# Kernel tuning notes

Hardware: AMD Instinct MI355X
Metric: run time of the kernel (lower is better)

Reference implementation:

```python
import jax, jax.numpy as jnp
import numpy as np

DIM = 384
NUM_HEADS = 8
HEAD_DIM = DIM // NUM_HEADS
SCALE = HEAD_DIM ** -0.5
MLP_HIDDEN = int(DIM * 4.0)
EPS = 1e-6


def setup_inputs() -> dict:
    key = jax.random.key(0)
    ks = jax.random.split(key, 8)
    s = 0.02
    return {
        "x": jax.random.normal(ks[0], (2, DIM, 8, 16, 16), dtype=jnp.float32),
        "g1": jnp.ones((DIM,), jnp.float32),
        "b1": jnp.zeros((DIM,), jnp.float32),
        "Wqkv": jax.random.normal(ks[1], (DIM, 3 * DIM), jnp.float32) * s,  # no bias (qkv_bias=False)
        "Wo": jax.random.normal(ks[2], (DIM, DIM), jnp.float32) * s,
        "bo": jnp.zeros((DIM,), jnp.float32),
        "g2": jnp.ones((DIM,), jnp.float32),
        "b2": jnp.zeros((DIM,), jnp.float32),
        "W1": jax.random.normal(ks[3], (DIM, MLP_HIDDEN), jnp.float32) * s,
        "b1m": jnp.zeros((MLP_HIDDEN,), jnp.float32),
        "W2": jax.random.normal(ks[4], (MLP_HIDDEN, DIM), jnp.float32) * s,
        "b2m": jnp.zeros((DIM,), jnp.float32),
    }


def _layernorm(x, g, b):
    mu = jnp.mean(x, axis=-1, keepdims=True)
    var = jnp.mean(jnp.square(x - mu), axis=-1, keepdims=True)
    return (x - mu) * jax.lax.rsqrt(var + EPS) * g + b


def _attention(h, Wqkv, Wo, bo):
    B, N, C = h.shape
    qkv = h @ Wqkv  # [B, N, 3C]
    qkv = qkv.reshape(B, N, 3, NUM_HEADS, HEAD_DIM).transpose(2, 0, 3, 1, 4)
    q, k, v = qkv[0], qkv[1], qkv[2]  # each [B, H, N, d]
    att = jax.nn.softmax(jnp.einsum('bhxd,bhyd->bhxy', q, k) * SCALE, axis=-1)
    out = jnp.einsum('bhxy,bhyd->bhxd', att, v)  # [B, H, N, d]
    out = out.transpose(0, 2, 1, 3).reshape(B, N, C)
    return out @ Wo + bo


def reference(x, g1, b1, Wqkv, Wo, bo, g2, b2, W1, b1m, W2, b2m):
    B, C, D, H, W = x.shape
    h = x.transpose(0, 2, 3, 4, 1).reshape(B, D * H * W, C)  # b (d h w) c
    h = h + _attention(_layernorm(h, g1, b1), Wqkv, Wo, bo)
    m = _layernorm(h, g2, b2)
    m = jax.nn.gelu(m @ W1 + b1m, approximate=False) @ W2 + b2m
    h = h + m
    return h.reshape(B, D, H, W, C).transpose(0, 4, 1, 2, 3)
```

## Files before the change

### kernel.cpp

```cpp
#include <hip/hip_runtime.h>
#include <hip/hip_bf16.h>
#include <math.h>

#define DIM    384
#define NHEAD  8
#define HDIM   48
#define NTOK   2048
#define BATCH  2
#define TOKS   (BATCH * NTOK)
#define HIDDEN 1536

typedef __bf16 bf16x8 __attribute__((ext_vector_type(8)));
typedef float  f32x4  __attribute__((ext_vector_type(4)));
typedef unsigned short u16;

union bfu { __hip_bfloat16 h; u16 u; };

__device__ __forceinline__ void load_lds16(const void* g, void* l) {
    __builtin_amdgcn_global_load_lds(
        (const __attribute__((address_space(1))) void*)g,
        (__attribute__((address_space(3))) void*)l, 16, 0, 0);
}

__global__ __launch_bounds__(256) void prep(
    const float* __restrict__ Wqkv, const float* __restrict__ Wo,
    const float* __restrict__ W1,   const float* __restrict__ W2,
    __hip_bfloat16* __restrict__ WqkvT, __hip_bfloat16* __restrict__ WoT,
    __hip_bfloat16* __restrict__ W1T,   __hip_bfloat16* __restrict__ W2T,
    const float* __restrict__ x, const float* __restrict__ g,
    const float* __restrict__ bta,
    float* __restrict__ hOut, __hip_bfloat16* __restrict__ y) {
    __shared__ __align__(16) char smem[384 * 33 * 4];
    int id = blockIdx.x;
    int tid = threadIdx.x;
    if (id < 1728) {
        float (*t)[33] = (float(*)[33])smem;
        const float* src; __hip_bfloat16* dst; int R, C;
        if (id < 432)       { src = Wqkv; dst = WqkvT; R = 384;  C = 1152; }
        else if (id < 576)  { id -= 432;  src = Wo;    dst = WoT;  R = 384;  C = 384; }
        else if (id < 1152) { id -= 576;  src = W1;    dst = W1T;  R = 384;  C = 1536; }
        else                { id -= 1152; src = W2;    dst = W2T;  R = 1536; C = 384; }
        int tc = C / 32;
        int i0 = (id / tc) * 32, j0 = (id % tc) * 32;
        int tx = tid & 31, ty = tid >> 5;
#pragma unroll
        for (int k = 0; k < 32; k += 8)
            t[ty + k][tx] = src[(size_t)(i0 + ty + k) * C + j0 + tx];
        __syncthreads();
#pragma unroll
        for (int k = 0; k < 32; k += 8)
            dst[(size_t)(j0 + ty + k) * R + i0 + tx] = __float2bfloat16(t[tx][ty + k]);
    } else {
        float* t = (float*)smem;
        int id2 = id - 1728;
        int n0 = (id2 & 63) * 32, b = id2 >> 6;
        const float* xb = x + (size_t)b * DIM * NTOK;
        for (int idx = tid; idx < 384 * 32; idx += 256) {
            int c = idx >> 5, n = idx & 31;
            t[c * 33 + n] = xb[(size_t)c * NTOK + n0 + n];
        }
        __syncthreads();
        int wid = tid >> 6, lane = tid & 63;
#pragma unroll
        for (int it = 0; it < 8; ++it) {
            int tl = it * 4 + wid;
            float v[6];
            float s = 0.f;
#pragma unroll
            for (int i = 0; i < 6; ++i) { v[i] = t[(lane + 64 * i) * 33 + tl]; s += v[i]; }
#pragma unroll
            for (int o = 32; o; o >>= 1) s += __shfl_xor(s, o, 64);
            float mu = s * (1.f / DIM);
            float s2 = 0.f;
#pragma unroll
            for (int i = 0; i < 6; ++i) { float d = v[i] - mu; s2 += d * d; }
#pragma unroll
            for (int o = 32; o; o >>= 1) s2 += __shfl_xor(s2, o, 64);
            float r = rsqrtf(s2 * (1.f / DIM) + 1e-6f);
            size_t tok = (size_t)b * NTOK + n0 + tl;
#pragma unroll
            for (int i = 0; i < 6; ++i) {
                int c = lane + 64 * i;
                hOut[tok * DIM + c] = v[i];
                y[tok * DIM + c] = __float2bfloat16((v[i] - mu) * r * g[c] + bta[c]);
            }
        }
    }
}

__global__ __launch_bounds__(256) void ln_kernel(const float* __restrict__ x,
                                                 const float* __restrict__ g,
                                                 const float* __restrict__ bta,
                                                 __hip_bfloat16* __restrict__ y) {
    int wid = threadIdx.x >> 6, lane = threadIdx.x & 63;
    int tok = blockIdx.x * 4 + wid;
    const float* xr = x + (size_t)tok * DIM;
    float v[6];
    float s = 0.f;
#pragma unroll
    for (int i = 0; i < 6; ++i) { v[i] = xr[lane + 64 * i]; s += v[i]; }
#pragma unroll
    for (int o = 32; o; o >>= 1) s += __shfl_xor(s, o, 64);
    float mu = s * (1.f / DIM);
    float s2 = 0.f;
#pragma unroll
    for (int i = 0; i < 6; ++i) { float d = v[i] - mu; s2 += d * d; }
#pragma unroll
    for (int o = 32; o; o >>= 1) s2 += __shfl_xor(s2, o, 64);
    float r = rsqrtf(s2 * (1.f / DIM) + 1e-6f);
    __hip_bfloat16* yr = y + (size_t)tok * DIM;
#pragma unroll
    for (int i = 0; i < 6; ++i) {
        int c = lane + 64 * i;
        yr[c] = __float2bfloat16((v[i] - mu) * r * g[c] + bta[c]);
    }
}

template<bool GELU, bool BF16OUT, bool TRANSOUT, bool QKV>
__global__ __launch_bounds__(256) void gemm_mfma(
    const __hip_bfloat16* __restrict__ A,
    const __hip_bfloat16* __restrict__ BT,
    const float* __restrict__ bias,
    const float* __restrict__ res,
    void* __restrict__ Cout,
    int M, int N, int K,
    __hip_bfloat16* __restrict__ vtout) {
    __shared__ __align__(16) u16 As[2][64 * 32];
    __shared__ __align__(16) u16 Bs[2][64 * 32];
    int bm = blockIdx.y * 64, bn = blockIdx.x * 64;
    int tid = threadIdx.x;
    int w = tid >> 6, l = tid & 63;
    int m0 = (w >> 1) * 32, n0 = (w & 1) * 32;
    int lm = l & 15, ksel = l >> 4;

    int row = tid >> 2, c16 = tid & 3;
    const __hip_bfloat16* ga = A  + (size_t)(bm + row) * K + c16 * 8;
    const __hip_bfloat16* gb = BT + (size_t)(bn + row) * K + c16 * 8;

    f32x4 acc[2][2] = {};
    for (int k0 = 0; k0 < K; k0 += 64) {
        load_lds16(ga + k0,      &As[0][tid * 8]);
        load_lds16(ga + k0 + 32, &As[1][tid * 8]);
        load_lds16(gb + k0,      &Bs[0][tid * 8]);
        load_lds16(gb + k0 + 32, &Bs[1][tid * 8]);
        __syncthreads();
#pragma unroll
        for (int kk = 0; kk < 2; ++kk) {
            bf16x8 af0 = *(const bf16x8*)&As[kk][(m0 +      lm) * 32 + ksel * 8];
            bf16x8 af1 = *(const bf16x8*)&As[kk][(m0 + 16 + lm) * 32 + ksel * 8];
            bf16x8 bf0 = *(const bf16x8*)&Bs[kk][(n0 +      lm) * 32 + ksel * 8];
            bf16x8 bf1 = *(const bf16x8*)&Bs[kk][(n0 + 16 + lm) * 32 + ksel * 8];
            acc[0][0] = __builtin_amdgcn_mfma_f32_16x16x32_bf16(af0, bf0, acc[0][0], 0, 0, 0);
            acc[0][1] = __builtin_amdgcn_mfma_f32_16x16x32_bf16(af0, bf1, acc[0][1], 0, 0, 0);
            acc[1][0] = __builtin_amdgcn_mfma_f32_16x16x32_bf16(af1, bf0, acc[1][0], 0, 0, 0);
            acc[1][1] = __builtin_amdgcn_mfma_f32_16x16x32_bf16(af1, bf1, acc[1][1], 0, 0, 0);
        }
        __syncthreads();
    }

    if constexpr (TRANSOUT) {
        __shared__ float ct[64 * 65];
#pragma unroll
        for (int i = 0; i < 2; ++i)
#pragma unroll
            for (int j = 0; j < 2; ++j)
#pragma unroll
                for (int r = 0; r < 4; ++r) {
                    int ml = m0 + i * 16 + ksel * 4 + r;
                    int cl = n0 + j * 16 + lm;
                    float v = acc[i][j][r];
                    if (bias) v += bias[bn + cl];
                    if (res)  v += res[(size_t)(bm + ml) * N + bn + cl];
                    ct[ml * 65 + cl] = v;
                }
        __syncthreads();
        int bb = bm >> 11, nb = bm & (NTOK - 1);
        float* outp = (float*)Cout + (size_t)bb * DIM * NTOK + nb;
#pragma unroll
        for (int cl = w; cl < 64; cl += 4)
            outp[(size_t)(bn + cl) * NTOK + l] = ct[l * 65 + cl];
    } else {
#pragma unroll
        for (int i = 0; i < 2; ++i)
#pragma unroll
            for (int j = 0; j < 2; ++j)
#pragma unroll
                for (int r = 0; r < 4; ++r) {
                    int rg = bm + m0 + i * 16 + ksel * 4 + r;
                    int cg = bn + n0 + j * 16 + lm;
                    float v = acc[i][j][r];
                    if (bias) v += bias[cg];
                    if (GELU) v = 0.5f * v * (1.f + erff(v * 0.7071067811865475f));
                    if (res)  v += res[(size_t)rg * N + cg];
                    if constexpr (QKV) {
                        if (cg < 768) {
                            ((__hip_bfloat16*)Cout)[(size_t)rg * 1152 + cg] = __float2bfloat16(v);
                        } else {
                            int c = cg - 768, hh = c / 48, dd = c - hh * 48;
                            int bb = rg >> 11, n = rg & (NTOK - 1);
                            int kk = n & 127;
                            int pos = ((kk >> 6) << 6) + ((kk & 15) << 2) + ((kk >> 4) & 3);
                            vtout[((size_t)(bb * NHEAD + hh) * 48 + dd) * 2048
                                  + (n & ~127) + pos] = __float2bfloat16(v);
                        }
                    } else if constexpr (BF16OUT) {
                        ((__hip_bfloat16*)Cout)[(size_t)rg * N + cg] = __float2bfloat16(v);
                    } else {
                        ((float*)Cout)[(size_t)rg * N + cg] = v;
                    }
                }
    }
}

#define ATK 128
#define PSTR 136
__global__ __launch_bounds__(512, 6) void attn_mfma(
    const u16* __restrict__ qkv,
    const u16* __restrict__ vt,
    __hip_bfloat16* __restrict__ outp) {
    __shared__ __align__(16) u16 PQ[64 * PSTR];
    __shared__ __align__(16) u16 Ks[128 * 72];
    __shared__ __align__(16) u16 Vs[48 * PSTR];
    const int q0 = blockIdx.x * 64;
    const int h = blockIdx.y, b = blockIdx.z;
    const int tid = threadIdx.x;
    const int w = tid >> 6, l = tid & 63, lm = l & 15, quad = l >> 4;
    const int qc = w >> 1, kh = w & 1;

    for (int idx = tid; idx < 128; idx += 512) {
        int r = idx >> 1, c = idx & 1;
        *(uint4*)&PQ[r * 72 + 48 + c * 8] = uint4{0, 0, 0, 0};
    }
    for (int idx = tid; idx < 256; idx += 512) {
        int r = idx >> 1, c = idx & 1;
        *(uint4*)&Ks[r * 72 + 48 + c * 8] = uint4{0, 0, 0, 0};
    }
    const u16* qbase = qkv + (size_t)(b * NTOK + q0) * 1152 + h * 48;
    for (int idx = tid; idx < 384; idx += 512) {
        int r = idx / 6, c = idx % 6;
        *(uint4*)&PQ[r * 72 + c * 8] = *(const uint4*)(qbase + (size_t)r * 1152 + c * 8);
    }
    __syncthreads();

    bf16x8 aq0 = *(const bf16x8*)&PQ[(qc * 16 + lm) * 72 +  0 + quad * 8];
    bf16x8 aq1 = *(const bf16x8*)&PQ[(qc * 16 + lm) * 72 + 32 + quad * 8];

    float l_i[4] = {0.f, 0.f, 0.f, 0.f};
    f32x4 o_acc[3] = {};

    const u16* kbase = qkv + (size_t)(b * NTOK) * 1152 + 384 + h * 48;
    const u16* vbase = vt + (size_t)(b * NHEAD + h) * 48 * 2048;
    const float sc2 = 0.14433756729740643f * 1.4426950408889634f;

    for (int kt = 0; kt < NTOK / ATK; ++kt) {
        __syncthreads();
#pragma unroll
        for (int idx = tid; idx < 768; idx += 512) {
            int r = idx / 6, c = idx % 6;
            *(uint4*)&Ks[r * 72 + c * 8] =
                *(const uint4*)(kbase + (size_t)(kt * ATK + r) * 1152 + c * 8);
        }
#pragma unroll
        for (int idx = tid; idx < 768; idx += 512) {
            int d = idx >> 4, c = idx & 15;
            *(uint4*)&Vs[d * PSTR + c * 8] =
                *(const uint4*)(vbase + (size_t)d * 2048 + kt * ATK + c * 8);
        }
        __syncthreads();

        f32x4 s[4];
#pragma unroll
        for (int ntp = 0; ntp < 4; ++ntp) {
            int nt = kh * 4 + ntp;
            bf16x8 kf0 = *(const bf16x8*)&Ks[(nt * 16 + lm) * 72 +  0 + quad * 8];
            bf16x8 kf1 = *(const bf16x8*)&Ks[(nt * 16 + lm) * 72 + 32 + quad * 8];
            f32x4 t = {};
            t = __builtin_amdgcn_mfma_f32_16x16x32_bf16(aq0, kf0, t, 0, 0, 0);
            t = __builtin_amdgcn_mfma_f32_16x16x32_bf16(aq1, kf1, t, 0, 0, 0);
            s[ntp] = t;
        }

#pragma unroll
        for (int r = 0; r < 4; ++r) {
            u16 pr[4];
#pragma unroll
            for (int ntp = 0; ntp < 4; ++ntp) {
                float p = exp2f(s[ntp][r] * sc2);
                l_i[r] += p;
                bfu cv; cv.h = __float2bfloat16(p);
                pr[ntp] = cv.u;
            }
            *(uint2*)&PQ[(qc * 16 + quad * 4 + r) * PSTR + kh * 64 + lm * 4] =
                *(const uint2*)pr;
        }

#pragma unroll
        for (int ksp = 0; ksp < 2; ++ksp) {
            int ks = kh * 2 + ksp;
            bf16x8 pf = *(const bf16x8*)&PQ[(qc * 16 + lm) * PSTR + ks * 32 + quad * 8];
#pragma unroll
            for (int nt = 0; nt < 3; ++nt) {
                bf16x8 vf = *(const bf16x8*)&Vs[(nt * 16 + lm) * PSTR + ks * 32 + quad * 8];
                o_acc[nt] = __builtin_amdgcn_mfma_f32_16x16x32_bf16(pf, vf, o_acc[nt], 0, 0, 0);
            }
        }
    }

    __syncthreads();
    float* red = (float*)Ks;
    if (kh == 1) {
        f32x4* base = (f32x4*)&red[(qc * 64 + l) * 16];
        base[0] = o_acc[0]; base[1] = o_acc[1]; base[2] = o_acc[2];
        f32x4 lv; lv[0] = l_i[0]; lv[1] = l_i[1]; lv[2] = l_i[2]; lv[3] = l_i[3];
        base[3] = lv;
    }
    __syncthreads();
    if (kh == 0) {
        f32x4* base = (f32x4*)&red[(qc * 64 + l) * 16];
        o_acc[0] += base[0]; o_acc[1] += base[1]; o_acc[2] += base[2];
        f32x4 lv = base[3];
#pragma unroll
        for (int r = 0; r < 4; ++r) {
            float lsum = l_i[r] + lv[r];
#pragma unroll
            for (int o = 8; o; o >>= 1) lsum += __shfl_xor(lsum, o, 64);
            float inv = 1.f / lsum;
#pragma unroll
            for (int nt = 0; nt < 3; ++nt)
                outp[(size_t)(b * NTOK + q0 + qc * 16 + quad * 4 + r) * DIM
                     + h * 48 + nt * 16 + lm]
                    = __float2bfloat16(o_acc[nt][r] * inv);
        }
    }
}

extern "C" void kernel_launch(void* const* d_in, const int* in_sizes, int n_in,
                              void* d_out, int out_size, void* d_ws, size_t ws_size,
                              hipStream_t stream) {
    const float* x    = (const float*)d_in[0];
    const float* g1   = (const float*)d_in[1];
    const float* b1   = (const float*)d_in[2];
    const float* Wqkv = (const float*)d_in[3];
    const float* Wo   = (const float*)d_in[4];
    const float* bo   = (const float*)d_in[5];
    const float* g2   = (const float*)d_in[6];
    const float* b2   = (const float*)d_in[7];
    const float* W1   = (const float*)d_in[8];
    const float* b1m  = (const float*)d_in[9];
    const float* W2   = (const float*)d_in[10];
    const float* b2m  = (const float*)d_in[11];
    float* out = (float*)d_out;

    char* p = (char*)d_ws;
    float* bufH = (float*)p;                       p += (size_t)TOKS * DIM * 4;
    char* qkvp = p;
    __hip_bfloat16* bufQKVb = (__hip_bfloat16*)p;  p += (size_t)TOKS * 3 * DIM * 2;
    __hip_bfloat16* bufVT   = (__hip_bfloat16*)p;  p += (size_t)TOKS * DIM * 2;
    __hip_bfloat16* bufNb   = (__hip_bfloat16*)p;  p += (size_t)TOKS * DIM * 2;
    __hip_bfloat16* bufAb   = (__hip_bfloat16*)p;  p += (size_t)TOKS * DIM * 2;
    __hip_bfloat16* WqkvT   = (__hip_bfloat16*)p;  p += (size_t)3 * DIM * DIM * 2;
    __hip_bfloat16* WoT     = (__hip_bfloat16*)p;  p += (size_t)DIM * DIM * 2;
    __hip_bfloat16* W1T     = (__hip_bfloat16*)p;  p += (size_t)HIDDEN * DIM * 2;
    __hip_bfloat16* W2T     = (__hip_bfloat16*)p;  p += (size_t)DIM * HIDDEN * 2;
    __hip_bfloat16* bufHIDb = (__hip_bfloat16*)qkvp;

    prep<<<1728 + 128, 256, 0, stream>>>(Wqkv, Wo, W1, W2, WqkvT, WoT, W1T, W2T,
                                         x, g1, b1, bufH, bufNb);
    gemm_mfma<false, true, false, true><<<dim3(3 * DIM / 64, TOKS / 64), 256, 0, stream>>>(
        bufNb, WqkvT, nullptr, nullptr, bufQKVb, TOKS, 3 * DIM, DIM, bufVT);
    attn_mfma<<<dim3(NTOK / 64, NHEAD, BATCH), 512, 0, stream>>>(
        (const u16*)bufQKVb, (const u16*)bufVT, bufAb);
    gemm_mfma<false, false, false, false><<<dim3(DIM / 64, TOKS / 64), 256, 0, stream>>>(
        bufAb, WoT, bo, bufH, bufH, TOKS, DIM, DIM, nullptr);
    ln_kernel<<<TOKS / 4, 256, 0, stream>>>(bufH, g2, b2, bufNb);
    gemm_mfma<true, true, false, false><<<dim3(HIDDEN / 64, TOKS / 64), 256, 0, stream>>>(
        bufNb, W1T, b1m, nullptr, bufHIDb, TOKS, HIDDEN, DIM, nullptr);
    gemm_mfma<false, false, true, false><<<dim3(DIM / 64, TOKS / 64), 256, 0, stream>>>(
        bufHIDb, W2T, b2m, bufH, out, TOKS, DIM, HIDDEN, nullptr);
}
```

Before: 197.6 us.

## Add 128x128-tile MFMA GEMM for QKV and MLP-up projections

Introduces a gemm128 kernel with 128x128 output tiles per 256-thread block, where each wave computes a 64x64 sub-tile with a 4x4 array of MFMA accumulators. It loads A and B into XOR-swizzled LDS using direct global-to-LDS loads. The QKV projection and the GELU MLP-up projection now use it instead of the 64x64 kernel, raising data reuse per LDS load. The trade-off is fewer blocks (e.g. 9x32 for QKV), more registers per thread, and a single-buffered loop with no prefetch overlap.

```diff
diff --git a/kernel.cpp b/kernel.cpp
--- a/kernel.cpp
+++ b/kernel.cpp
@@ -212,6 +212,89 @@
     }
 }
 
+template<bool GELU, bool QKV>
+__global__ __launch_bounds__(256) void gemm128(
+    const __hip_bfloat16* __restrict__ A,
+    const __hip_bfloat16* __restrict__ BT,
+    const float* __restrict__ bias,
+    void* __restrict__ Cout,
+    int M, int N, int K,
+    __hip_bfloat16* __restrict__ vtout) {
+    __shared__ __align__(16) u16 As[128 * 64];
+    __shared__ __align__(16) u16 Bs[128 * 64];
+    const int bm = blockIdx.y * 128, bn = blockIdx.x * 128;
+    const int tid = threadIdx.x;
+    const int w = tid >> 6, l = tid & 63;
+    const int wr = w >> 1, wc = w & 1;
+    const int lm = l & 15, quad = l >> 4;
+
+    const int g = (tid & 7) ^ ((tid >> 3) & 7);
+    const __hip_bfloat16* ga0 = A  + (size_t)(bm + (tid >> 3)) * K + g * 8;
+    const __hip_bfloat16* gb0 = BT + (size_t)(bn + (tid >> 3)) * K + g * 8;
+
+    const int xorv = (lm & 7) << 4;
+    f32x4 acc[4][4] = {};
+
+    for (int k0 = 0; k0 < K; k0 += 64) {
+#pragma unroll
+        for (int i = 0; i < 4; ++i) {
+            load_lds16(ga0 + (size_t)i * 32 * K + k0, (char*)As + tid * 16 + i * 4096);
+            load_lds16(gb0 + (size_t)i * 32 * K + k0, (char*)Bs + tid * 16 + i * 4096);
+        }
+        __syncthreads();
+#pragma unroll
+        for (int kk = 0; kk < 2; ++kk) {
+            bf16x8 af[4], bf[4];
+#pragma unroll
+            for (int m = 0; m < 4; ++m) {
+                int row = wr * 64 + m * 16 + lm;
+                af[m] = *(const bf16x8*)((const char*)As + row * 128
+                                         + ((((kk * 4 + quad) << 4)) ^ xorv));
+            }
+#pragma unroll
+            for (int n = 0; n < 4; ++n) {
+                int row = wc * 64 + n * 16 + lm;
+                bf[n] = *(const bf16x8*)((const char*)Bs + row * 128
+                                         + ((((kk * 4 + quad) << 4)) ^ xorv));
+            }
+#pragma unroll
+            for (int m = 0; m < 4; ++m)
+#pragma unroll
+                for (int n = 0; n < 4; ++n)
+                    acc[m][n] = __builtin_amdgcn_mfma_f32_16x16x32_bf16(
+                        af[m], bf[n], acc[m][n], 0, 0, 0);
+        }
+        __syncthreads();
+    }
+
+#pragma unroll
+    for (int m = 0; m < 4; ++m)
+#pragma unroll
+        for (int n = 0; n < 4; ++n)
+#pragma unroll
+            for (int r = 0; r < 4; ++r) {
+                int rg = bm + wr * 64 + m * 16 + quad * 4 + r;
+                int cg = bn + wc * 64 + n * 16 + lm;
+                float v = acc[m][n][r];
+                if (bias) v += bias[cg];
+                if (GELU) v = 0.5f * v * (1.f + erff(v * 0.7071067811865475f));
+                if constexpr (QKV) {
+                    if (cg < 768) {
+                        ((__hip_bfloat16*)Cout)[(size_t)rg * 1152 + cg] = __float2bfloat16(v);
+                    } else {
+                        int c = cg - 768, hh = c / 48, dd = c - hh * 48;
+                        int bb = rg >> 11, nn = rg & (NTOK - 1);
+                        int kk = nn & 127;
+                        int pos = ((kk >> 6) << 6) + ((kk & 15) << 2) + ((kk >> 4) & 3);
+                        vtout[((size_t)(bb * NHEAD + hh) * 48 + dd) * 2048
+                              + (nn & ~127) + pos] = __float2bfloat16(v);
+                    }
+                } else {
+                    ((__hip_bfloat16*)Cout)[(size_t)rg * N + cg] = __float2bfloat16(v);
+                }
+            }
+}
+
 #define ATK 128
 #define PSTR 136
 __global__ __launch_bounds__(512, 6) void attn_mfma(
@@ -366,15 +449,15 @@
 
     prep<<<1728 + 128, 256, 0, stream>>>(Wqkv, Wo, W1, W2, WqkvT, WoT, W1T, W2T,
                                          x, g1, b1, bufH, bufNb);
-    gemm_mfma<false, true, false, true><<<dim3(3 * DIM / 64, TOKS / 64), 256, 0, stream>>>(
-        bufNb, WqkvT, nullptr, nullptr, bufQKVb, TOKS, 3 * DIM, DIM, bufVT);
+    gemm128<false, true><<<dim3(3 * DIM / 128, TOKS / 128), 256, 0, stream>>>(
+        bufNb, WqkvT, nullptr, bufQKVb, TOKS, 3 * DIM, DIM, bufVT);
     attn_mfma<<<dim3(NTOK / 64, NHEAD, BATCH), 512, 0, stream>>>(
         (const u16*)bufQKVb, (const u16*)bufVT, bufAb);
     gemm_mfma<false, false, false, false><<<dim3(DIM / 64, TOKS / 64), 256, 0, stream>>>(
         bufAb, WoT, bo, bufH, bufH, TOKS, DIM, DIM, nullptr);
     ln_kernel<<<TOKS / 4, 256, 0, stream>>>(bufH, g2, b2, bufNb);
-    gemm_mfma<true, true, false, false><<<dim3(HIDDEN / 64, TOKS / 64), 256, 0, stream>>>(
-        bufNb, W1T, b1m, nullptr, bufHIDb, TOKS, HIDDEN, DIM, nullptr);
+    gemm128<true, false><<<dim3(HIDDEN / 128, TOKS / 128), 256, 0, stream>>>(
+        bufNb, W1T, b1m, bufHIDb, TOKS, HIDDEN, DIM, nullptr);
     gemm_mfma<false, false, true, false><<<dim3(DIM / 64, TOKS / 64), 256, 0, stream>>>(
         bufHIDb, W2T, b2m, bufH, out, TOKS, DIM, HIDDEN, nullptr);
 }
```

Result: slower. 213.5 us (+8.1%).

## Prefetch next K/V tile into registers and swizzle workgroup order for L2 locality

Applied to the files above, without the earlier changes.

The attention kernel now loads the next K and V tile into registers while the current tile is being computed, then stores them to LDS at the start of the next iteration, so global load latency overlaps with MFMA work. Both the GEMM and attention kernels remap block IDs with a stride-8 swizzle, likely to spread neighbouring tiles across XCDs or to improve L2 reuse. The attention occupancy hint drops from 6 to 4 waves per SIMD to leave room for the extra prefetch registers, at the cost of lower occupancy.

```diff
diff --git a/kernel.cpp b/kernel.cpp
--- a/kernel.cpp
+++ b/kernel.cpp
@@ -127,7 +127,11 @@
     __hip_bfloat16* __restrict__ vtout) {
     __shared__ __align__(16) u16 As[2][64 * 32];
     __shared__ __align__(16) u16 Bs[2][64 * 32];
-    int bm = blockIdx.y * 64, bn = blockIdx.x * 64;
+    const int nwg = gridDim.x * gridDim.y;
+    const int lid = blockIdx.y * gridDim.x + blockIdx.x;
+    const int swz = (lid & 7) * (nwg >> 3) + (lid >> 3);
+    const int bx = swz % gridDim.x, by = swz / gridDim.x;
+    int bm = by * 64, bn = bx * 64;
     int tid = threadIdx.x;
     int w = tid >> 6, l = tid & 63;
     int m0 = (w >> 1) * 32, n0 = (w & 1) * 32;
@@ -214,15 +218,17 @@
 
 #define ATK 128
 #define PSTR 136
-__global__ __launch_bounds__(512, 6) void attn_mfma(
+__global__ __launch_bounds__(512, 4) void attn_mfma(
     const u16* __restrict__ qkv,
     const u16* __restrict__ vt,
     __hip_bfloat16* __restrict__ outp) {
     __shared__ __align__(16) u16 PQ[64 * PSTR];
     __shared__ __align__(16) u16 Ks[128 * 72];
     __shared__ __align__(16) u16 Vs[48 * PSTR];
-    const int q0 = blockIdx.x * 64;
-    const int h = blockIdx.y, b = blockIdx.z;
+    const int lid = (blockIdx.z * NHEAD + blockIdx.y) * (NTOK / 64) + blockIdx.x;
+    const int swz = (lid & 7) * 64 + (lid >> 3);
+    const int q0 = (swz & 31) * 64;
+    const int h = (swz >> 5) & 7, b = swz >> 8;
     const int tid = threadIdx.x;
     const int w = tid >> 6, l = tid & 63, lm = l & 15, quad = l >> 4;
     const int qc = w >> 1, kh = w & 1;
@@ -252,21 +258,41 @@
     const u16* vbase = vt + (size_t)(b * NHEAD + h) * 48 * 2048;
     const float sc2 = 0.14433756729740643f * 1.4426950408889634f;
 
+    const int kr0 = tid / 6,  kc0 = tid % 6;
+    const int kr1 = (tid + 512) / 6, kc1 = (tid + 512) % 6;
+    const int vd0 = tid >> 4, vc0 = tid & 15;
+    const int vd1 = (tid + 512) >> 4, vc1 = (tid + 512) & 15;
+    const bool two = tid < 256;
+    uint4 kp0, kp1, vp0, vp1;
+
+    {
+        kp0 = *(const uint4*)(kbase + (size_t)kr0 * 1152 + kc0 * 8);
+        vp0 = *(const uint4*)(vbase + (size_t)vd0 * 2048 + vc0 * 8);
+        if (two) {
+            kp1 = *(const uint4*)(kbase + (size_t)kr1 * 1152 + kc1 * 8);
+            vp1 = *(const uint4*)(vbase + (size_t)vd1 * 2048 + vc1 * 8);
+        }
+    }
+
     for (int kt = 0; kt < NTOK / ATK; ++kt) {
         __syncthreads();
-#pragma unroll
-        for (int idx = tid; idx < 768; idx += 512) {
-            int r = idx / 6, c = idx % 6;
-            *(uint4*)&Ks[r * 72 + c * 8] =
-                *(const uint4*)(kbase + (size_t)(kt * ATK + r) * 1152 + c * 8);
-        }
-#pragma unroll
-        for (int idx = tid; idx < 768; idx += 512) {
-            int d = idx >> 4, c = idx & 15;
-            *(uint4*)&Vs[d * PSTR + c * 8] =
-                *(const uint4*)(vbase + (size_t)d * 2048 + kt * ATK + c * 8);
-        }
-        __syncthreads();
+        *(uint4*)&Ks[kr0 * 72 + kc0 * 8] = kp0;
+        *(uint4*)&Vs[vd0 * PSTR + vc0 * 8] = vp0;
+        if (two) {
+            *(uint4*)&Ks[kr1 * 72 + kc1 * 8] = kp1;
+            *(uint4*)&Vs[vd1 * PSTR + vc1 * 8] = vp1;
+        }
+        __syncthreads();
+        if (kt + 1 < NTOK / ATK) {
+            const u16* kb = kbase + (size_t)(kt + 1) * ATK * 1152;
+            const u16* vb = vbase + (size_t)(kt + 1) * ATK;
+            kp0 = *(const uint4*)(kb + (size_t)kr0 * 1152 + kc0 * 8);
+            vp0 = *(const uint4*)(vb + (size_t)vd0 * 2048 + vc0 * 8);
+            if (two) {
+                kp1 = *(const uint4*)(kb + (size_t)kr1 * 1152 + kc1 * 8);
+                vp1 = *(const uint4*)(vb + (size_t)vd1 * 2048 + vc1 * 8);
+            }
+        }
 
         f32x4 s[4];
 #pragma unroll
```

Result: no change. 194.4 us (-1.6%).
